# Kernel optimization log

Hardware: AMD Instinct MI355X
Metric: run time of the kernel (lower is better)

## Reference

```python
import jax, jax.numpy as jnp
import numpy as np

C = 64
DQ = C // 8  # query/key channel dim


def setup_inputs() -> dict:
    key = jax.random.key(0)
    ks = jax.random.split(key, 8)
    B, H, W = 8, 64, 64
    x = jax.random.normal(ks[0], (B, C, H, W), dtype=jnp.float32)
    # 1x1 conv weights stored as [out, in] matrices (kernel dims squeezed)
    wq = jax.random.normal(ks[1], (DQ, C), dtype=jnp.float32) * 0.05
    bq = jax.random.normal(ks[2], (DQ,), dtype=jnp.float32) * 0.05
    wk = jax.random.normal(ks[3], (DQ, C), dtype=jnp.float32) * 0.05
    bk = jax.random.normal(ks[4], (DQ,), dtype=jnp.float32) * 0.05
    wv = jax.random.normal(ks[5], (C, C), dtype=jnp.float32) * 0.05
    bv = jax.random.normal(ks[6], (C,), dtype=jnp.float32) * 0.05
    gamma = jax.random.normal(ks[7], (1,), dtype=jnp.float32)
    return {"x": x, "wq": wq, "bq": bq, "wk": wk, "bk": bk,
            "wv": wv, "bv": bv, "gamma": gamma}


def reference(x, wq, bq, wk, bk, wv, bv, gamma):
    B, Cc, H, W = x.shape
    N = H * W
    xf = x.reshape(B, Cc, N)                      # [B, C, N]
    # 1x1 convs == channel matmuls
    q = jnp.einsum('dc,bcn->bdn', wq, xf) + bq[None, :, None]   # [B, DQ, N]
    k = jnp.einsum('dc,bcn->bdn', wk, xf) + bk[None, :, None]   # [B, DQ, N]
    v = jnp.einsum('oc,bcn->bon', wv, xf) + bv[None, :, None]   # [B, C, N]
    # energy[b, m, n] = sum_d q[b, d, m] * k[b, d, n]
    energy = jnp.einsum('bdm,bdn->bmn', q, k)                   # [B, N, N]
    attention = jax.nn.softmax(energy, axis=-1)
    # out[b, c, m] = sum_n v[b, c, n] * attention[b, m, n]
    out = jnp.einsum('bcn,bmn->bcm', v, attention).reshape(B, Cc, H, W)
    return gamma[0] * out + x
```

## Files before the change

kernel.cpp:

```cpp
#include <hip/hip_runtime.h>
#include <math.h>

#define NTOK 4096
#define CCH  64
#define LOG2E 1.4426950408889634f
#define NSPLIT 4

typedef __attribute__((ext_vector_type(8)))  short bf16x8;
typedef __attribute__((ext_vector_type(4)))  float f32x4;
typedef __attribute__((ext_vector_type(16))) float f32x16;
typedef __attribute__((ext_vector_type(2)))  unsigned int uint32x2;

__device__ __forceinline__ unsigned short f2bf_rne(float f) {
    unsigned int u = __float_as_uint(f);
    u += 0x7FFFu + ((u >> 16) & 1u);
    return (unsigned short)(u >> 16);
}
__device__ __forceinline__ float bf2f(unsigned short u) {
    return __uint_as_float(((unsigned int)u) << 16);
}

__global__ __launch_bounds__(256) void proj_kernel(
    const float* __restrict__ x,
    const float* __restrict__ wq, const float* __restrict__ bq,
    const float* __restrict__ wk, const float* __restrict__ bk,
    const float* __restrict__ wv, const float* __restrict__ bv,
    unsigned short* __restrict__ qt, unsigned short* __restrict__ kt,
    unsigned short* __restrict__ vbf)
{
    __shared__ unsigned short xsb[64 * 68];
    __shared__ unsigned short wa[80 * 68];
    __shared__ unsigned short vtmp[64 * 66];
    __shared__ float bb[80];

    const int t  = threadIdx.x;
    const int b  = blockIdx.x >> 6;
    const int n0 = (blockIdx.x & 63) << 6;

    const int lane = t & 63;
    const int w    = t >> 6;
    const int l15  = lane & 15;
    const int g    = lane >> 4;

    {
        const int n  = t & 63;
        const int c0 = t >> 6;
        #pragma unroll
        for (int r = 0; r < 16; ++r) {
            const int c = c0 + 4 * r;
            xsb[n * 68 + c] = f2bf_rne(x[((size_t)(b * CCH + c)) * NTOK + n0 + n]);
        }
    }
    #pragma unroll
    for (int r = 0; r < 16; ++r) {
        const int i = t + 256 * r;
        wa[(i >> 6) * 68 + (i & 63)] = f2bf_rne(wv[i]);
    }
    {
        const int i0 = t, i1 = t + 256;
        wa[(64 + (i0 >> 6)) * 68 + (i0 & 63)] = f2bf_rne(wq[i0] * LOG2E);
        wa[(64 + (i1 >> 6)) * 68 + (i1 & 63)] = f2bf_rne(wq[i1] * LOG2E);
        wa[(72 + (i0 >> 6)) * 68 + (i0 & 63)] = f2bf_rne(wk[i0]);
        wa[(72 + (i1 >> 6)) * 68 + (i1 & 63)] = f2bf_rne(wk[i1]);
    }
    if (t < 80) {
        float bias;
        if (t < 64)      bias = bv[t];
        else if (t < 72) bias = bq[t - 64] * LOG2E;
        else             bias = bk[t - 72];
        bb[t] = bias;
    }
    __syncthreads();

    f32x4 acc[5];
    #pragma unroll
    for (int mt = 0; mt < 5; ++mt) acc[mt] = (f32x4){0.f, 0.f, 0.f, 0.f};
    #pragma unroll
    for (int kc = 0; kc < 2; ++kc) {
        const bf16x8 bx = *(const bf16x8*)&xsb[(w * 16 + l15) * 68 + kc * 32 + g * 8];
        #pragma unroll
        for (int mt = 0; mt < 5; ++mt) {
            const bf16x8 aw = *(const bf16x8*)&wa[(mt * 16 + l15) * 68 + kc * 32 + g * 8];
            acc[mt] = __builtin_amdgcn_mfma_f32_16x16x32_bf16(aw, bx, acc[mt], 0, 0, 0);
        }
    }

    const int n = w * 16 + l15;
    #pragma unroll
    for (int mt = 0; mt < 4; ++mt) {
        #pragma unroll
        for (int r = 0; r < 4; ++r) {
            const int c = mt * 16 + g * 4 + r;
            vtmp[c * 66 + 4 * l15 + w] = f2bf_rne(acc[mt][r] + bb[c]);
        }
    }
    {
        unsigned short vals[4];
        #pragma unroll
        for (int r = 0; r < 4; ++r)
            vals[r] = f2bf_rne(acc[4][r] + bb[64 + g * 4 + r]);
        const unsigned int lo = (unsigned int)vals[0] | ((unsigned int)vals[1] << 16);
        const unsigned int hi = (unsigned int)vals[2] | ((unsigned int)vals[3] << 16);
        unsigned short* dst = ((g < 2) ? qt : kt) +
                              ((size_t)(b * NTOK + n0 + n)) * 8 + (g & 1) * 4;
        *(uint32x2*)dst = (uint32x2){lo, hi};
    }
    __syncthreads();

    {
        const int c = t >> 2;
        const int q = t & 3;
        unsigned short* dst = vbf + ((size_t)(b * CCH + c)) * NTOK + n0 + q * 16;
        *(bf16x8*)dst       = *(const bf16x8*)&vtmp[c * 66 + q * 16];
        *(bf16x8*)(dst + 8) = *(const bf16x8*)&vtmp[c * 66 + q * 16 + 8];
    }
}

__global__ __launch_bounds__(256, 6) void attn_kernel(
    const unsigned short* __restrict__ qt, const unsigned short* __restrict__ kt,
    const unsigned short* __restrict__ vbf,
    unsigned short* __restrict__ opart, float* __restrict__ lpart, int B)
{
    __shared__ unsigned short vs[64 * 88];
    __shared__ unsigned short ps[64 * 88];

    const int t    = threadIdx.x;
    const int lane = t & 63;
    const int w    = t >> 6;
    const int bid  = blockIdx.x;
    const int b    = bid % B;
    const int p    = (bid / B) % NSPLIT;
    const int m0   = (bid / (B * NSPLIT)) << 6;

    const int l15 = lane & 15;
    const int g   = lane >> 4;
    const int l31 = lane & 31;
    const int h   = lane >> 5;

    const int NIT     = 64 / NSPLIT;
    const int itStart = p * NIT;

    bf16x8 a_q = {};
    if (g == 0)
        a_q = *(const bf16x8*)&qt[((size_t)(b * NTOK + m0 + w * 16 + l15)) * 8];

    const int c0  = t >> 3, seg = t & 7;
    const int c1  = c0 + 32;
    const unsigned short* vsrc0 = vbf + ((size_t)(b * CCH + c0)) * NTOK
                                      + itStart * 64 + seg * 8;
    const unsigned short* vsrc1 = vbf + ((size_t)(b * CCH + c1)) * NTOK
                                      + itStart * 64 + seg * 8;
    unsigned short* vdst0 = &vs[c0 * 88 + seg * 8];
    unsigned short* vdst1 = &vs[c1 * 88 + seg * 8];

    const unsigned short* ksrc = kt + ((size_t)(b * NTOK + itStart * 64 + l15)) * 8;

    bf16x8 vreg0 = *(const bf16x8*)vsrc0;
    bf16x8 vreg1 = *(const bf16x8*)vsrc1;
    bf16x8 kr0 = {}, kr1 = {}, kr2 = {}, kr3 = {};
    if (g == 0) {
        kr0 = *(const bf16x8*)(ksrc);
        kr1 = *(const bf16x8*)(ksrc + 128);
        kr2 = *(const bf16x8*)(ksrc + 256);
        kr3 = *(const bf16x8*)(ksrc + 384);
    }

    f32x16 oacc;
    #pragma unroll
    for (int i = 0; i < 16; ++i) oacc[i] = 0.f;
    float rs0 = 0.f, rs1 = 0.f, rs2 = 0.f, rs3 = 0.f;

    const int crow = ((w >> 1) * 32 + l31) * 88;
    const int mrow = ((w & 1) * 32 + l31) * 88;

    for (int it = 0; it < NIT; ++it) {
        __syncthreads();

        *(bf16x8*)vdst0 = vreg0;
        *(bf16x8*)vdst1 = vreg1;

        const f32x4 z = {0.f, 0.f, 0.f, 0.f};
        f32x4 s0 = __builtin_amdgcn_mfma_f32_16x16x32_bf16(a_q, kr0, z, 0, 0, 0);
        f32x4 s1 = __builtin_amdgcn_mfma_f32_16x16x32_bf16(a_q, kr1, z, 0, 0, 0);
        f32x4 s2 = __builtin_amdgcn_mfma_f32_16x16x32_bf16(a_q, kr2, z, 0, 0, 0);
        f32x4 s3 = __builtin_amdgcn_mfma_f32_16x16x32_bf16(a_q, kr3, z, 0, 0, 0);

        if (it + 1 < NIT) {
            vsrc0 += 64;  vsrc1 += 64;  ksrc += 64 * 8;
            vreg0 = *(const bf16x8*)vsrc0;
            vreg1 = *(const bf16x8*)vsrc1;
            if (g == 0) {
                kr0 = *(const bf16x8*)(ksrc);
                kr1 = *(const bf16x8*)(ksrc + 128);
                kr2 = *(const bf16x8*)(ksrc + 256);
                kr3 = *(const bf16x8*)(ksrc + 384);
            }
        }

        #pragma unroll
        for (int r = 0; r < 4; ++r) {
            const float p0 = __builtin_amdgcn_exp2f(s0[r]);
            const float p1 = __builtin_amdgcn_exp2f(s1[r]);
            const float p2 = __builtin_amdgcn_exp2f(s2[r]);
            const float p3 = __builtin_amdgcn_exp2f(s3[r]);
            const unsigned int lo = __builtin_amdgcn_perm(
                __float_as_uint(p1), __float_as_uint(p0), 0x07060302u);
            const unsigned int hi = __builtin_amdgcn_perm(
                __float_as_uint(p3), __float_as_uint(p2), 0x07060302u);
            *(uint32x2*)&ps[(w * 16 + g * 4 + r) * 88 + 4 * l15] = (uint32x2){lo, hi};
            const float ssum = (p0 + p1) + (p2 + p3);
            if      (r == 0) rs0 += ssum;
            else if (r == 1) rs1 += ssum;
            else if (r == 2) rs2 += ssum;
            else             rs3 += ssum;
        }
        __syncthreads();

        #pragma unroll
        for (int kc = 0; kc < 4; ++kc) {
            const bf16x8 a_v = *(const bf16x8*)&vs[crow + kc * 16 + h * 8];
            const bf16x8 b_p = *(const bf16x8*)&ps[mrow + kc * 16 + h * 8];
            oacc = __builtin_amdgcn_mfma_f32_32x32x16_bf16(a_v, b_p, oacc, 0, 0, 0);
        }
    }

    #pragma unroll
    for (int xm = 1; xm <= 8; xm <<= 1) {
        rs0 += __shfl_xor(rs0, xm);
        rs1 += __shfl_xor(rs1, xm);
        rs2 += __shfl_xor(rs2, xm);
        rs3 += __shfl_xor(rs3, xm);
    }
    if (l15 == 0) {
        float* lp = lpart + (size_t)(p * B + b) * NTOK + m0 + w * 16 + g * 4;
        lp[0] = rs0; lp[1] = rs1; lp[2] = rs2; lp[3] = rs3;
    }
    {
        const int mloc = (w & 1) * 32 + l31;
        #pragma unroll
        for (int reg = 0; reg < 16; ++reg) {
            const int c = (w >> 1) * 32 + (reg & 3) + 8 * (reg >> 2) + 4 * h;
            opart[((size_t)((p * B + b) * CCH + c)) * NTOK + m0 + mloc] =
                f2bf_rne(oacc[reg]);
        }
    }
}

__global__ __launch_bounds__(256) void combine_kernel(
    const unsigned short* __restrict__ opart, const float* __restrict__ lpart,
    const float* __restrict__ x, const float* __restrict__ gamma_p,
    float* __restrict__ out, int B)
{
    const float  gm      = gamma_p[0];
    const size_t nf4     = (size_t)B * CCH * NTOK / 4;
    const size_t ostride = (size_t)B * CCH * NTOK;
    for (size_t f = (size_t)blockIdx.x * 256 + threadIdx.x; f < nf4;
         f += (size_t)gridDim.x * 256) {
        const int m4 = ((int)(f & 1023)) * 4;
        const int bc = (int)(f >> 10);
        const int bi = bc >> 6;
        const size_t obase = (size_t)bc * NTOK + m4;

        float4 osum = {0.f, 0.f, 0.f, 0.f};
        float4 lsum = {0.f, 0.f, 0.f, 0.f};
        #pragma unroll
        for (int p = 0; p < NSPLIT; ++p) {
            const ushort4 o = *(const ushort4*)&opart[obase + (size_t)p * ostride];
            const float4  l = *(const float4*)&lpart[(size_t)(p * B + bi) * NTOK + m4];
            osum.x += bf2f(o.x); osum.y += bf2f(o.y);
            osum.z += bf2f(o.z); osum.w += bf2f(o.w);
            lsum.x += l.x; lsum.y += l.y; lsum.z += l.z; lsum.w += l.w;
        }
        const float4 xv = *(const float4*)&x[obase];
        float4 r;
        r.x = osum.x * gm / lsum.x + xv.x;
        r.y = osum.y * gm / lsum.y + xv.y;
        r.z = osum.z * gm / lsum.z + xv.z;
        r.w = osum.w * gm / lsum.w + xv.w;
        *(float4*)&out[obase] = r;
    }
}

extern "C" void kernel_launch(void* const* d_in, const int* in_sizes, int n_in,
                              void* d_out, int out_size, void* d_ws, size_t ws_size,
                              hipStream_t stream) {
    const float* x     = (const float*)d_in[0];
    const float* wq    = (const float*)d_in[1];
    const float* bq    = (const float*)d_in[2];
    const float* wk    = (const float*)d_in[3];
    const float* bk    = (const float*)d_in[4];
    const float* wv    = (const float*)d_in[5];
    const float* bv    = (const float*)d_in[6];
    const float* gamma = (const float*)d_in[7];
    float* out = (float*)d_out;

    int B = in_sizes[0] / (CCH * NTOK);

    unsigned short* wsp   = (unsigned short*)d_ws;
    unsigned short* qt    = wsp;
    unsigned short* kt    = qt + (size_t)B * NTOK * 8;
    unsigned short* vbf   = kt + (size_t)B * NTOK * 8;
    unsigned short* opart = vbf + (size_t)B * CCH * NTOK;
    float*          lpart = (float*)(opart + (size_t)NSPLIT * B * CCH * NTOK);

    proj_kernel<<<B * 64, 256, 0, stream>>>(x, wq, bq, wk, bk, wv, bv, qt, kt, vbf);
    attn_kernel<<<NSPLIT * B * 64, 256, 0, stream>>>(qt, kt, vbf, opart, lpart, B);
    combine_kernel<<<512, 256, 0, stream>>>(opart, lpart, x, gamma, out, B);
}
```

Before: 125.5 us.

## Load V fragments directly into registers and double-buffer P in LDS

V fragments for the PV MFMA now come straight from global memory into registers, so the V staging through LDS goes away. The P tile is double-buffered, which lets one of the two per-iteration barriers be dropped. s_setprio is raised around the MFMA sections. Each wave now loads V redundantly: waves that share a channel half read the same data, which raises global/L2 traffic. The V loads are also issued after the MFMA with less lead time, so their latency may be exposed.

```diff
diff --git a/kernel.cpp b/kernel.cpp
--- a/kernel.cpp
+++ b/kernel.cpp
@@ -121,8 +121,7 @@
     const unsigned short* __restrict__ vbf,
     unsigned short* __restrict__ opart, float* __restrict__ lpart, int B)
 {
-    __shared__ unsigned short vs[64 * 88];
-    __shared__ unsigned short ps[64 * 88];
+    __shared__ unsigned short ps[2][64 * 88];
 
     const int t    = threadIdx.x;
     const int lane = t & 63;
@@ -144,19 +143,16 @@
     if (g == 0)
         a_q = *(const bf16x8*)&qt[((size_t)(b * NTOK + m0 + w * 16 + l15)) * 8];
 
-    const int c0  = t >> 3, seg = t & 7;
-    const int c1  = c0 + 32;
-    const unsigned short* vsrc0 = vbf + ((size_t)(b * CCH + c0)) * NTOK
-                                      + itStart * 64 + seg * 8;
-    const unsigned short* vsrc1 = vbf + ((size_t)(b * CCH + c1)) * NTOK
-                                      + itStart * 64 + seg * 8;
-    unsigned short* vdst0 = &vs[c0 * 88 + seg * 8];
-    unsigned short* vdst1 = &vs[c1 * 88 + seg * 8];
+    const int cv = (w >> 1) * 32 + l31;
+    const unsigned short* vp = vbf + ((size_t)(b * CCH + cv)) * NTOK
+                                   + itStart * 64 + h * 8;
 
     const unsigned short* ksrc = kt + ((size_t)(b * NTOK + itStart * 64 + l15)) * 8;
 
-    bf16x8 vreg0 = *(const bf16x8*)vsrc0;
-    bf16x8 vreg1 = *(const bf16x8*)vsrc1;
+    bf16x8 av0 = *(const bf16x8*)(vp);
+    bf16x8 av1 = *(const bf16x8*)(vp + 16);
+    bf16x8 av2 = *(const bf16x8*)(vp + 32);
+    bf16x8 av3 = *(const bf16x8*)(vp + 48);
     bf16x8 kr0 = {}, kr1 = {}, kr2 = {}, kr3 = {};
     if (g == 0) {
         kr0 = *(const bf16x8*)(ksrc);
@@ -170,25 +166,21 @@
     for (int i = 0; i < 16; ++i) oacc[i] = 0.f;
     float rs0 = 0.f, rs1 = 0.f, rs2 = 0.f, rs3 = 0.f;
 
-    const int crow = ((w >> 1) * 32 + l31) * 88;
     const int mrow = ((w & 1) * 32 + l31) * 88;
 
     for (int it = 0; it < NIT; ++it) {
-        __syncthreads();
-
-        *(bf16x8*)vdst0 = vreg0;
-        *(bf16x8*)vdst1 = vreg1;
+        unsigned short* psc = &ps[it & 1][0];
 
         const f32x4 z = {0.f, 0.f, 0.f, 0.f};
+        __builtin_amdgcn_s_setprio(1);
         f32x4 s0 = __builtin_amdgcn_mfma_f32_16x16x32_bf16(a_q, kr0, z, 0, 0, 0);
         f32x4 s1 = __builtin_amdgcn_mfma_f32_16x16x32_bf16(a_q, kr1, z, 0, 0, 0);
         f32x4 s2 = __builtin_amdgcn_mfma_f32_16x16x32_bf16(a_q, kr2, z, 0, 0, 0);
         f32x4 s3 = __builtin_amdgcn_mfma_f32_16x16x32_bf16(a_q, kr3, z, 0, 0, 0);
+        __builtin_amdgcn_s_setprio(0);
 
         if (it + 1 < NIT) {
-            vsrc0 += 64;  vsrc1 += 64;  ksrc += 64 * 8;
-            vreg0 = *(const bf16x8*)vsrc0;
-            vreg1 = *(const bf16x8*)vsrc1;
+            ksrc += 64 * 8;
             if (g == 0) {
                 kr0 = *(const bf16x8*)(ksrc);
                 kr1 = *(const bf16x8*)(ksrc + 128);
@@ -207,7 +199,7 @@
                 __float_as_uint(p1), __float_as_uint(p0), 0x07060302u);
             const unsigned int hi = __builtin_amdgcn_perm(
                 __float_as_uint(p3), __float_as_uint(p2), 0x07060302u);
-            *(uint32x2*)&ps[(w * 16 + g * 4 + r) * 88 + 4 * l15] = (uint32x2){lo, hi};
+            *(uint32x2*)&psc[(w * 16 + g * 4 + r) * 88 + 4 * l15] = (uint32x2){lo, hi};
             const float ssum = (p0 + p1) + (p2 + p3);
             if      (r == 0) rs0 += ssum;
             else if (r == 1) rs1 += ssum;
@@ -216,11 +208,25 @@
         }
         __syncthreads();
 
-        #pragma unroll
-        for (int kc = 0; kc < 4; ++kc) {
-            const bf16x8 a_v = *(const bf16x8*)&vs[crow + kc * 16 + h * 8];
-            const bf16x8 b_p = *(const bf16x8*)&ps[mrow + kc * 16 + h * 8];
-            oacc = __builtin_amdgcn_mfma_f32_32x32x16_bf16(a_v, b_p, oacc, 0, 0, 0);
+        __builtin_amdgcn_s_setprio(1);
+        {
+            const bf16x8 bp0 = *(const bf16x8*)&psc[mrow + 0 * 16 + h * 8];
+            oacc = __builtin_amdgcn_mfma_f32_32x32x16_bf16(av0, bp0, oacc, 0, 0, 0);
+            const bf16x8 bp1 = *(const bf16x8*)&psc[mrow + 1 * 16 + h * 8];
+            oacc = __builtin_amdgcn_mfma_f32_32x32x16_bf16(av1, bp1, oacc, 0, 0, 0);
+            const bf16x8 bp2 = *(const bf16x8*)&psc[mrow + 2 * 16 + h * 8];
+            oacc = __builtin_amdgcn_mfma_f32_32x32x16_bf16(av2, bp2, oacc, 0, 0, 0);
+            const bf16x8 bp3 = *(const bf16x8*)&psc[mrow + 3 * 16 + h * 8];
+            oacc = __builtin_amdgcn_mfma_f32_32x32x16_bf16(av3, bp3, oacc, 0, 0, 0);
+        }
+        __builtin_amdgcn_s_setprio(0);
+
+        if (it + 1 < NIT) {
+            vp += 64;
+            av0 = *(const bf16x8*)(vp);
+            av1 = *(const bf16x8*)(vp + 16);
+            av2 = *(const bf16x8*)(vp + 32);
+            av3 = *(const bf16x8*)(vp + 48);
         }
     }
 
```

New measurement: 347.9 us. 2.77x slower.

## Fuse split-K combine into attention kernel via last-arriving-block counter

Applied to the files above, without the earlier changes.

Removes the separate combine kernel. Each attention block bumps a per-tile atomic counter after writing its partial output and row sums. The last of the NSPLIT blocks for a tile reduces the partials, applies gamma and the residual, and writes the output. The counters are reset inside proj_kernel. This saves a kernel launch and a full-grid pass, at the cost of atomic stores and loads, a fence, and tail work done by only a quarter of the blocks.

```diff
diff --git a/kernel.cpp b/kernel.cpp
--- a/kernel.cpp
+++ b/kernel.cpp
@@ -26,7 +26,7 @@
     const float* __restrict__ wk, const float* __restrict__ bk,
     const float* __restrict__ wv, const float* __restrict__ bv,
     unsigned short* __restrict__ qt, unsigned short* __restrict__ kt,
-    unsigned short* __restrict__ vbf)
+    unsigned short* __restrict__ vbf, unsigned int* __restrict__ cnt)
 {
     __shared__ unsigned short xsb[64 * 68];
     __shared__ unsigned short wa[80 * 68];
@@ -41,6 +41,10 @@
     const int w    = t >> 6;
     const int l15  = lane & 15;
     const int g    = lane >> 4;
+
+    if (t == 0)
+        __hip_atomic_store(&cnt[blockIdx.x], 0u, __ATOMIC_RELAXED,
+                           __HIP_MEMORY_SCOPE_AGENT);
 
     {
         const int n  = t & 63;
@@ -119,10 +123,14 @@
 __global__ __launch_bounds__(256, 6) void attn_kernel(
     const unsigned short* __restrict__ qt, const unsigned short* __restrict__ kt,
     const unsigned short* __restrict__ vbf,
-    unsigned short* __restrict__ opart, float* __restrict__ lpart, int B)
+    unsigned short* __restrict__ opart, float* __restrict__ lpart,
+    const float* __restrict__ x, const float* __restrict__ gamma_p,
+    float* __restrict__ out, unsigned int* __restrict__ cnt, int B)
 {
     __shared__ unsigned short vs[64 * 88];
     __shared__ unsigned short ps[64 * 88];
+    __shared__ float lsc[64];
+    __shared__ int   winflag;
 
     const int t    = threadIdx.x;
     const int lane = t & 63;
@@ -233,51 +241,73 @@
     }
     if (l15 == 0) {
         float* lp = lpart + (size_t)(p * B + b) * NTOK + m0 + w * 16 + g * 4;
-        lp[0] = rs0; lp[1] = rs1; lp[2] = rs2; lp[3] = rs3;
+        __hip_atomic_store(&lp[0], rs0, __ATOMIC_RELAXED, __HIP_MEMORY_SCOPE_AGENT);
+        __hip_atomic_store(&lp[1], rs1, __ATOMIC_RELAXED, __HIP_MEMORY_SCOPE_AGENT);
+        __hip_atomic_store(&lp[2], rs2, __ATOMIC_RELAXED, __HIP_MEMORY_SCOPE_AGENT);
+        __hip_atomic_store(&lp[3], rs3, __ATOMIC_RELAXED, __HIP_MEMORY_SCOPE_AGENT);
     }
     {
         const int mloc = (w & 1) * 32 + l31;
         #pragma unroll
         for (int reg = 0; reg < 16; ++reg) {
             const int c = (w >> 1) * 32 + (reg & 3) + 8 * (reg >> 2) + 4 * h;
-            opart[((size_t)((p * B + b) * CCH + c)) * NTOK + m0 + mloc] =
-                f2bf_rne(oacc[reg]);
-        }
-    }
-}
-
-__global__ __launch_bounds__(256) void combine_kernel(
-    const unsigned short* __restrict__ opart, const float* __restrict__ lpart,
-    const float* __restrict__ x, const float* __restrict__ gamma_p,
-    float* __restrict__ out, int B)
-{
-    const float  gm      = gamma_p[0];
-    const size_t nf4     = (size_t)B * CCH * NTOK / 4;
-    const size_t ostride = (size_t)B * CCH * NTOK;
-    for (size_t f = (size_t)blockIdx.x * 256 + threadIdx.x; f < nf4;
-         f += (size_t)gridDim.x * 256) {
-        const int m4 = ((int)(f & 1023)) * 4;
-        const int bc = (int)(f >> 10);
-        const int bi = bc >> 6;
-        const size_t obase = (size_t)bc * NTOK + m4;
-
-        float4 osum = {0.f, 0.f, 0.f, 0.f};
-        float4 lsum = {0.f, 0.f, 0.f, 0.f};
-        #pragma unroll
-        for (int p = 0; p < NSPLIT; ++p) {
-            const ushort4 o = *(const ushort4*)&opart[obase + (size_t)p * ostride];
-            const float4  l = *(const float4*)&lpart[(size_t)(p * B + bi) * NTOK + m4];
-            osum.x += bf2f(o.x); osum.y += bf2f(o.y);
-            osum.z += bf2f(o.z); osum.w += bf2f(o.w);
-            lsum.x += l.x; lsum.y += l.y; lsum.z += l.z; lsum.w += l.w;
-        }
-        const float4 xv = *(const float4*)&x[obase];
+            __hip_atomic_store(
+                &opart[((size_t)((p * B + b) * CCH + c)) * NTOK + m0 + mloc],
+                f2bf_rne(oacc[reg]), __ATOMIC_RELAXED, __HIP_MEMORY_SCOPE_AGENT);
+        }
+    }
+
+    __syncthreads();
+    if (t == 0) {
+        __threadfence();
+        const unsigned int old = __hip_atomic_fetch_add(
+            &cnt[b * 64 + (m0 >> 6)], 1u,
+            __ATOMIC_RELAXED, __HIP_MEMORY_SCOPE_AGENT);
+        winflag = (old == 3u);
+    }
+    __syncthreads();
+    if (!winflag) return;
+
+    const float gm = gamma_p[0];
+    if (t < 64) {
+        float s = 0.f;
+        #pragma unroll
+        for (int pp = 0; pp < NSPLIT; ++pp)
+            s += __hip_atomic_load(
+                &lpart[(size_t)(pp * B + b) * NTOK + m0 + t],
+                __ATOMIC_RELAXED, __HIP_MEMORY_SCOPE_AGENT);
+        lsc[t] = gm / s;
+    }
+    __syncthreads();
+
+    const int cc = t >> 2, tq = t & 3;
+    float acc2[16];
+    #pragma unroll
+    for (int j = 0; j < 16; ++j) acc2[j] = 0.f;
+    #pragma unroll
+    for (int pp = 0; pp < NSPLIT; ++pp) {
+        const unsigned long long* src = (const unsigned long long*)
+            &opart[((size_t)((pp * B + b) * CCH + cc)) * NTOK + m0 + tq * 16];
+        #pragma unroll
+        for (int q = 0; q < 4; ++q) {
+            const unsigned long long v = __hip_atomic_load(
+                src + q, __ATOMIC_RELAXED, __HIP_MEMORY_SCOPE_AGENT);
+            acc2[q * 4 + 0] += bf2f((unsigned short)(v));
+            acc2[q * 4 + 1] += bf2f((unsigned short)(v >> 16));
+            acc2[q * 4 + 2] += bf2f((unsigned short)(v >> 32));
+            acc2[q * 4 + 3] += bf2f((unsigned short)(v >> 48));
+        }
+    }
+    const size_t rowo = ((size_t)(b * CCH + cc)) * NTOK + m0 + tq * 16;
+    #pragma unroll
+    for (int q = 0; q < 4; ++q) {
+        const float4 xv = *(const float4*)&x[rowo + q * 4];
         float4 r;
-        r.x = osum.x * gm / lsum.x + xv.x;
-        r.y = osum.y * gm / lsum.y + xv.y;
-        r.z = osum.z * gm / lsum.z + xv.z;
-        r.w = osum.w * gm / lsum.w + xv.w;
-        *(float4*)&out[obase] = r;
+        r.x = acc2[q * 4 + 0] * lsc[tq * 16 + q * 4 + 0] + xv.x;
+        r.y = acc2[q * 4 + 1] * lsc[tq * 16 + q * 4 + 1] + xv.y;
+        r.z = acc2[q * 4 + 2] * lsc[tq * 16 + q * 4 + 2] + xv.z;
+        r.w = acc2[q * 4 + 3] * lsc[tq * 16 + q * 4 + 3] + xv.w;
+        *(float4*)&out[rowo + q * 4] = r;
     }
 }
 
@@ -302,8 +332,10 @@
     unsigned short* vbf   = kt + (size_t)B * NTOK * 8;
     unsigned short* opart = vbf + (size_t)B * CCH * NTOK;
     float*          lpart = (float*)(opart + (size_t)NSPLIT * B * CCH * NTOK);
-
-    proj_kernel<<<B * 64, 256, 0, stream>>>(x, wq, bq, wk, bk, wv, bv, qt, kt, vbf);
-    attn_kernel<<<NSPLIT * B * 64, 256, 0, stream>>>(qt, kt, vbf, opart, lpart, B);
-    combine_kernel<<<512, 256, 0, stream>>>(opart, lpart, x, gamma, out, B);
-}
+    unsigned int*   cnt   = (unsigned int*)(lpart + (size_t)NSPLIT * B * NTOK);
+
+    proj_kernel<<<B * 64, 256, 0, stream>>>(x, wq, bq, wk, bk, wv, bv,
+                                            qt, kt, vbf, cnt);
+    attn_kernel<<<NSPLIT * B * 64, 256, 0, stream>>>(qt, kt, vbf, opart, lpart,
+                                                     x, gamma, out, cnt, B);
+}
```

New measurement: 432.6 us. 245% more time.
